# Kernel optimization log

Hardware: AMD Instinct MI355X
Metric: run time of the kernel (lower is better)

The kernel has to match this reference:

```python
import jax, jax.numpy as jnp
import numpy as np

N_NODES = 100000
D_FEAT = 128
N_EDGES = 1500000
H1 = 2 * D_FEAT  # 256, input to first linear (concat of src/dst feats)
H2 = 128


def setup_inputs() -> dict:
    key = jax.random.key(0)
    k_x, k_e, k_w1, k_w2 = jax.random.split(key, 4)
    x = jax.random.normal(k_x, (N_NODES, D_FEAT), dtype=jnp.float32)
    edge_label_index = jax.random.randint(k_e, (2, N_EDGES), 0, N_NODES, dtype=jnp.int64)
    # Kaiming-ish small init for stability
    W1 = jax.random.normal(k_w1, (H1, H2), dtype=jnp.float32) * (1.0 / np.sqrt(H1))
    b1 = jnp.zeros((H2,), dtype=jnp.float32)
    W2 = jax.random.normal(k_w2, (H2, 1), dtype=jnp.float32) * (1.0 / np.sqrt(H2))
    b2 = jnp.zeros((1,), dtype=jnp.float32)
    return {"x": x, "edge_label_index": edge_label_index,
            "W1": W1, "b1": b1, "W2": W2, "b2": b2}


def reference(x, edge_label_index, W1, b1, W2, b2):
    row, col = edge_label_index[0], edge_label_index[1]
    # gather node pair features and concat: [E, 2*D]
    h = jnp.concatenate([x[row], x[col]], axis=-1)
    h = jax.nn.relu(h @ W1 + b1)  # [E, H2]
    out = h @ W2 + b2             # [E, 1]
    return out.reshape(-1)        # [E]
```

## Files before the change

### kernel.cpp

```cpp
#include <hip/hip_runtime.h>
#include <hip/hip_bf16.h>
#include <stdint.h>

typedef __attribute__((ext_vector_type(8))) short s16x8;
typedef __attribute__((ext_vector_type(8))) unsigned short u16x8;
typedef __attribute__((ext_vector_type(4))) float f32x4;

#define D_FEAT 128
#define H2 128
#define BLOCK_THREADS 512
#define WAVES 8
#define MW 32
#define EDGES_PER_BLOCK (WAVES * MW)

__device__ __forceinline__ unsigned short f2bf(float f) {
  uint32_t u = __float_as_uint(f);
  return (unsigned short)((u + 0x7fffu + ((u >> 16) & 1u)) >> 16);
}

__global__ void k_cvt_x(const float* __restrict__ x, unsigned short* __restrict__ xb, int n8) {
  int i = blockIdx.x * blockDim.x + threadIdx.x;
  if (i >= n8) return;
  const f32x4* p = (const f32x4*)x + (size_t)i * 2;
  f32x4 a = p[0], b = p[1];
  u16x8 o;
  o[0] = f2bf(a[0]); o[1] = f2bf(a[1]); o[2] = f2bf(a[2]); o[3] = f2bf(a[3]);
  o[4] = f2bf(b[0]); o[5] = f2bf(b[1]); o[6] = f2bf(b[2]); o[7] = f2bf(b[3]);
  ((u16x8*)xb)[i] = o;
}

__global__ void k_cvt_w1(const float* __restrict__ W1, unsigned short* __restrict__ w1t) {
  int tid = blockIdx.x * blockDim.x + threadIdx.x;
  int chunk = tid >> 7;
  int n = tid & 127;
  u16x8 o;
#pragma unroll
  for (int j = 0; j < 8; ++j)
    o[j] = f2bf(W1[(chunk * 8 + j) * H2 + n]);
  *(u16x8*)(w1t + (n << 8) + ((chunk ^ (n & 7)) << 3)) = o;
}

template <bool XBF>
__global__ __launch_bounds__(BLOCK_THREADS, 4)
void k_edge_mlp(const float* __restrict__ xf,
                const unsigned short* __restrict__ xb,
                const int* __restrict__ eli,
                const float* __restrict__ W1,
                const unsigned short* __restrict__ w1ws,
                const float* __restrict__ b1,
                const float* __restrict__ W2,
                const float* __restrict__ b2,
                float* __restrict__ out, int E, int nNodes)
{
  __shared__ unsigned short w1t[H2 * 256];
  const int t    = threadIdx.x;
  const int lane = t & 63;
  const int wid  = t >> 6;
  const int c    = lane & 15;
  const int g    = lane >> 4;

  if (XBF) {
#pragma unroll
    for (int i = 0; i < 8; ++i) {
      int idx = i * BLOCK_THREADS + t;
      ((u16x8*)w1t)[idx] = ((const u16x8*)w1ws)[idx];
    }
  } else {
    int cg = t >> 7;
    int n  = t & 127;
#pragma unroll
    for (int i = 0; i < 8; ++i) {
      int ch = cg + 4 * i;
      u16x8 o;
#pragma unroll
      for (int j = 0; j < 8; ++j)
        o[j] = f2bf(W1[(ch * 8 + j) * H2 + n]);
      *(u16x8*)(w1t + (n << 8) + ((ch ^ (n & 7)) << 3)) = o;
    }
  }

  const int wbase = blockIdx.x * EDGES_PER_BLOCK + wid * MW;
  const unsigned short* pr[2];
  const unsigned short* pc[2];
  const float* prf[2];
  const float* pcf[2];
#pragma unroll
  for (int m = 0; m < 2; ++m) {
    int e = wbase + m * 16 + c;
    e = e < E ? e : E - 1;
    int nr = eli[e];
    int nc = eli[E + e];
    nr = nr < 0 ? 0 : (nr >= nNodes ? nNodes - 1 : nr);
    nc = nc < 0 ? 0 : (nc >= nNodes ? nNodes - 1 : nc);
    if (XBF) {
      pr[m] = xb + (unsigned)nr * D_FEAT + g * 8;
      pc[m] = xb + (unsigned)nc * D_FEAT + g * 8;
    } else {
      prf[m] = xf + (unsigned)nr * D_FEAT + g * 8;
      pcf[m] = xf + (unsigned)nc * D_FEAT + g * 8;
    }
  }

  __syncthreads();

  auto loadA = [&](int kk, s16x8* dst) {
#pragma unroll
    for (int m = 0; m < 2; ++m) {
      if (XBF) {
        const unsigned short* p = (kk < 4 ? pr[m] : pc[m]);
        dst[m] = *(const s16x8*)(p + (kk & 3) * 32);
      } else {
        const float* p = (kk < 4 ? prf[m] : pcf[m]) + (kk & 3) * 32;
        const f32x4* q = (const f32x4*)p;
        f32x4 a = q[0], b = q[1];
        s16x8 v;
        v[0] = (short)f2bf(a[0]); v[1] = (short)f2bf(a[1]);
        v[2] = (short)f2bf(a[2]); v[3] = (short)f2bf(a[3]);
        v[4] = (short)f2bf(b[0]); v[5] = (short)f2bf(b[1]);
        v[6] = (short)f2bf(b[2]); v[7] = (short)f2bf(b[3]);
        dst[m] = v;
      }
    }
  };

  f32x4 acc[2][8];
#pragma unroll
  for (int m = 0; m < 2; ++m)
#pragma unroll
    for (int f = 0; f < 8; ++f) {
      f32x4 z = {0.f, 0.f, 0.f, 0.f};
      acc[m][f] = z;
    }

  s16x8 abuf[2][2];
  loadA(0, abuf[0]);
  loadA(1, abuf[1]);

#pragma unroll
  for (int kk = 0; kk < 8; ++kk) {
    __builtin_amdgcn_s_setprio(1);
#pragma unroll
    for (int f = 0; f < 8; ++f) {
      int n = f * 16 + c;
      s16x8 bfrag = *(const s16x8*)(w1t + (n << 8) + (((kk * 4 + g) ^ (n & 7)) << 3));
#pragma unroll
      for (int m = 0; m < 2; ++m)
        acc[m][f] = __builtin_amdgcn_mfma_f32_16x16x32_bf16(abuf[kk & 1][m], bfrag, acc[m][f], 0, 0, 0);
    }
    __builtin_amdgcn_s_setprio(0);
    if (kk < 6) loadA(kk + 2, abuf[kk & 1]);
  }

  float b1v[8], w2v[8];
#pragma unroll
  for (int f = 0; f < 8; ++f) {
    b1v[f] = b1[f * 16 + c];
    w2v[f] = W2[f * 16 + c];
  }
  const float b2s = b2[0];

#pragma unroll
  for (int m = 0; m < 2; ++m) {
    float sr[4];
#pragma unroll
    for (int r = 0; r < 4; ++r) {
      float s = 0.f;
#pragma unroll
      for (int f = 0; f < 8; ++f) {
        float h = acc[m][f][r] + b1v[f];
        h = h > 0.f ? h : 0.f;
        s += h * w2v[f];
      }
#pragma unroll
      for (int msk = 1; msk < 16; msk <<= 1)
        s += __shfl_xor(s, msk, 64);
      sr[r] = s;
    }
    int ebase = wbase + m * 16 + g * 4;
    if (c == 0 && ebase < E) {
      f32x4 o = {sr[0] + b2s, sr[1] + b2s, sr[2] + b2s, sr[3] + b2s};
      *(f32x4*)(out + ebase) = o;
    }
  }
}

extern "C" void kernel_launch(void* const* d_in, const int* in_sizes, int n_in,
                              void* d_out, int out_size, void* d_ws, size_t ws_size,
                              hipStream_t stream) {
  const float* x   = (const float*)d_in[0];
  const int*   eli = (const int*)d_in[1];
  const float* W1  = (const float*)d_in[2];
  const float* b1  = (const float*)d_in[3];
  const float* W2  = (const float*)d_in[4];
  const float* b2  = (const float*)d_in[5];
  float* out = (float*)d_out;

  const int E      = in_sizes[1] / 2;
  const int nNodes = in_sizes[0] / D_FEAT;

  const size_t xbytes = (size_t)nNodes * D_FEAT * 2;
  const size_t need   = xbytes + 65536;
  const bool bfpath   = (ws_size >= need);

  const int grid = (E + EDGES_PER_BLOCK - 1) / EDGES_PER_BLOCK;

  if (bfpath) {
    unsigned short* xbw  = (unsigned short*)d_ws;
    unsigned short* w1tw = (unsigned short*)((char*)d_ws + xbytes);
    int n8 = nNodes * D_FEAT / 8;
    k_cvt_x<<<(n8 + 255) / 256, 256, 0, stream>>>(x, xbw, n8);
    k_cvt_w1<<<16, 256, 0, stream>>>(W1, w1tw);
    k_edge_mlp<true><<<grid, BLOCK_THREADS, 0, stream>>>(
        x, xbw, eli, W1, w1tw, b1, W2, b2, out, E, nNodes);
  } else {
    k_edge_mlp<false><<<grid, BLOCK_THREADS, 0, stream>>>(
        x, nullptr, eli, W1, nullptr, b1, W2, b2, out, E, nNodes);
  }
}
```

Before: 140.7 us.

## Make edge MLP kernel persistent with cross-tile prefetch of gathered features

Launches a fixed grid of 512 blocks that loop over edge tiles in grid-stride order. W1 is staged into LDS once per block instead of once per tile. The next tile's indices and first feature fragments are prefetched while the current tile's epilogue runs. The B-fragment LDS offsets are precomputed into registers. This raises register pressure and may lower occupancy, and the fixed grid can leave CUs unevenly loaded.

```diff
diff --git a/kernel.cpp b/kernel.cpp
--- a/kernel.cpp
+++ b/kernel.cpp
@@ -11,7 +11,8 @@
 #define BLOCK_THREADS 512
 #define WAVES 8
 #define MW 32
-#define EDGES_PER_BLOCK (WAVES * MW)
+#define EPB (WAVES * MW)
+#define PERSIST_BLOCKS 512
 
 __device__ __forceinline__ unsigned short f2bf(float f) {
   uint32_t u = __float_as_uint(f);
@@ -53,21 +54,22 @@
                 float* __restrict__ out, int E, int nNodes)
 {
   __shared__ unsigned short w1t[H2 * 256];
-  const int t    = threadIdx.x;
-  const int lane = t & 63;
-  const int wid  = t >> 6;
+  const int t0   = threadIdx.x;
+  const int lane = t0 & 63;
+  const int wid  = t0 >> 6;
   const int c    = lane & 15;
   const int g    = lane >> 4;
+  const int ch7  = c & 7;
 
   if (XBF) {
 #pragma unroll
     for (int i = 0; i < 8; ++i) {
-      int idx = i * BLOCK_THREADS + t;
+      int idx = i * BLOCK_THREADS + t0;
       ((u16x8*)w1t)[idx] = ((const u16x8*)w1ws)[idx];
     }
   } else {
-    int cg = t >> 7;
-    int n  = t & 127;
+    int cg = t0 >> 7;
+    int n  = t0 & 127;
 #pragma unroll
     for (int i = 0; i < 8; ++i) {
       int ch = cg + 4 * i;
@@ -79,39 +81,40 @@
     }
   }
 
-  const int wbase = blockIdx.x * EDGES_PER_BLOCK + wid * MW;
-  const unsigned short* pr[2];
-  const unsigned short* pc[2];
-  const float* prf[2];
-  const float* pcf[2];
-#pragma unroll
-  for (int m = 0; m < 2; ++m) {
-    int e = wbase + m * 16 + c;
-    e = e < E ? e : E - 1;
-    int nr = eli[e];
-    int nc = eli[E + e];
-    nr = nr < 0 ? 0 : (nr >= nNodes ? nNodes - 1 : nr);
-    nc = nc < 0 ? 0 : (nc >= nNodes ? nNodes - 1 : nc);
-    if (XBF) {
-      pr[m] = xb + (unsigned)nr * D_FEAT + g * 8;
-      pc[m] = xb + (unsigned)nc * D_FEAT + g * 8;
-    } else {
-      prf[m] = xf + (unsigned)nr * D_FEAT + g * 8;
-      pcf[m] = xf + (unsigned)nc * D_FEAT + g * 8;
-    }
-  }
+  unsigned boff[8];
+#pragma unroll
+  for (int kk = 0; kk < 8; ++kk)
+    boff[kk] = (unsigned)(c * 256 + (((kk * 4 + g) ^ ch7) << 3));
 
   __syncthreads();
 
-  auto loadA = [&](int kk, s16x8* dst) {
+  const int nt = (E + EPB - 1) / EPB;
+  int t = blockIdx.x;
+  if (t >= nt) return;
+  const int stride = gridDim.x;
+
+  auto mkoff = [&](int tt, unsigned* ro, unsigned* co) {
 #pragma unroll
     for (int m = 0; m < 2; ++m) {
+      int e = tt * EPB + wid * MW + m * 16 + c;
+      e = e < E ? e : E - 1;
+      int nr = eli[e];
+      int nc = eli[E + e];
+      nr = nr < 0 ? 0 : (nr >= nNodes ? nNodes - 1 : nr);
+      nc = nc < 0 ? 0 : (nc >= nNodes ? nNodes - 1 : nc);
+      ro[m] = (unsigned)nr * D_FEAT + g * 8;
+      co[m] = (unsigned)nc * D_FEAT + g * 8;
+    }
+  };
+
+  auto loadA = [&](const unsigned* ro, const unsigned* co, int kk, s16x8* dst) {
+#pragma unroll
+    for (int m = 0; m < 2; ++m) {
+      unsigned off = (kk < 4 ? ro[m] : co[m]) + (unsigned)((kk & 3) * 32);
       if (XBF) {
-        const unsigned short* p = (kk < 4 ? pr[m] : pc[m]);
-        dst[m] = *(const s16x8*)(p + (kk & 3) * 32);
+        dst[m] = *(const s16x8*)(xb + off);
       } else {
-        const float* p = (kk < 4 ? prf[m] : pcf[m]) + (kk & 3) * 32;
-        const f32x4* q = (const f32x4*)p;
+        const f32x4* q = (const f32x4*)(xf + off);
         f32x4 a = q[0], b = q[1];
         s16x8 v;
         v[0] = (short)f2bf(a[0]); v[1] = (short)f2bf(a[1]);
@@ -123,64 +126,82 @@
     }
   };
 
-  f32x4 acc[2][8];
-#pragma unroll
-  for (int m = 0; m < 2; ++m)
+  unsigned ro[2], co[2], ron[2], con[2];
+  mkoff(t, ro, co);
+  s16x8 abuf[2][2];
+  loadA(ro, co, 0, abuf[0]);
+  loadA(ro, co, 1, abuf[1]);
+
+  while (true) {
+    const int tn = t + stride;
+    const bool more = (tn < nt);
+    if (more) mkoff(tn, ron, con);
+
+    f32x4 acc[2][8];
+#pragma unroll
+    for (int m = 0; m < 2; ++m)
+#pragma unroll
+      for (int f = 0; f < 8; ++f) {
+        f32x4 z = {0.f, 0.f, 0.f, 0.f};
+        acc[m][f] = z;
+      }
+
+#pragma unroll
+    for (int kk = 0; kk < 8; ++kk) {
+      __builtin_amdgcn_s_setprio(1);
+#pragma unroll
+      for (int f = 0; f < 8; ++f) {
+        s16x8 bfrag = *(const s16x8*)(w1t + boff[kk] + f * 4096);
+#pragma unroll
+        for (int m = 0; m < 2; ++m)
+          acc[m][f] = __builtin_amdgcn_mfma_f32_16x16x32_bf16(abuf[kk & 1][m], bfrag, acc[m][f], 0, 0, 0);
+      }
+      __builtin_amdgcn_s_setprio(0);
+      if (kk < 6) loadA(ro, co, kk + 2, abuf[kk & 1]);
+    }
+
+    if (more) {
+      loadA(ron, con, 0, abuf[0]);
+      loadA(ron, con, 1, abuf[1]);
+    }
+
+    float b1v[8], w2v[8];
 #pragma unroll
     for (int f = 0; f < 8; ++f) {
-      f32x4 z = {0.f, 0.f, 0.f, 0.f};
-      acc[m][f] = z;
-    }
-
-  s16x8 abuf[2][2];
-  loadA(0, abuf[0]);
-  loadA(1, abuf[1]);
-
-#pragma unroll
-  for (int kk = 0; kk < 8; ++kk) {
-    __builtin_amdgcn_s_setprio(1);
-#pragma unroll
-    for (int f = 0; f < 8; ++f) {
-      int n = f * 16 + c;
-      s16x8 bfrag = *(const s16x8*)(w1t + (n << 8) + (((kk * 4 + g) ^ (n & 7)) << 3));
-#pragma unroll
-      for (int m = 0; m < 2; ++m)
-        acc[m][f] = __builtin_amdgcn_mfma_f32_16x16x32_bf16(abuf[kk & 1][m], bfrag, acc[m][f], 0, 0, 0);
-    }
-    __builtin_amdgcn_s_setprio(0);
-    if (kk < 6) loadA(kk + 2, abuf[kk & 1]);
-  }
-
-  float b1v[8], w2v[8];
-#pragma unroll
-  for (int f = 0; f < 8; ++f) {
-    b1v[f] = b1[f * 16 + c];
-    w2v[f] = W2[f * 16 + c];
-  }
-  const float b2s = b2[0];
-
-#pragma unroll
-  for (int m = 0; m < 2; ++m) {
-    float sr[4];
-#pragma unroll
-    for (int r = 0; r < 4; ++r) {
-      float s = 0.f;
-#pragma unroll
-      for (int f = 0; f < 8; ++f) {
-        float h = acc[m][f][r] + b1v[f];
-        h = h > 0.f ? h : 0.f;
-        s += h * w2v[f];
-      }
-#pragma unroll
-      for (int msk = 1; msk < 16; msk <<= 1)
-        s += __shfl_xor(s, msk, 64);
-      sr[r] = s;
-    }
-    int ebase = wbase + m * 16 + g * 4;
-    if (c == 0 && ebase < E) {
-      f32x4 o = {sr[0] + b2s, sr[1] + b2s, sr[2] + b2s, sr[3] + b2s};
-      *(f32x4*)(out + ebase) = o;
-    }
+      b1v[f] = b1[f * 16 + c];
+      w2v[f] = W2[f * 16 + c];
+    }
+    const float b2s = b2[0];
+
+    const int tbase = t * EPB + wid * MW;
+#pragma unroll
+    for (int m = 0; m < 2; ++m) {
+      float sr[4];
+#pragma unroll
+      for (int r = 0; r < 4; ++r) {
+        float s = 0.f;
+#pragma unroll
+        for (int f = 0; f < 8; ++f) {
+          float h = acc[m][f][r] + b1v[f];
+          h = h > 0.f ? h : 0.f;
+          s += h * w2v[f];
+        }
+#pragma unroll
+        for (int msk = 1; msk < 16; msk <<= 1)
+          s += __shfl_xor(s, msk, 64);
+        sr[r] = s;
+      }
+      int ebase = tbase + m * 16 + g * 4;
+      if (c == 0 && ebase < E) {
+        f32x4 o = {sr[0] + b2s, sr[1] + b2s, sr[2] + b2s, sr[3] + b2s};
+        *(f32x4*)(out + ebase) = o;
+      }
+    }
+
+    if (!more) break;
+    t = tn;
+#pragma unroll
+    for (int m = 0; m < 2; ++m) { ro[m] = ron[m]; co[m] = con[m]; }
   }
 }
 
@@ -202,7 +223,8 @@
   const size_t need   = xbytes + 65536;
   const bool bfpath   = (ws_size >= need);
 
-  const int grid = (E + EDGES_PER_BLOCK - 1) / EDGES_PER_BLOCK;
+  const int nt   = (E + EPB - 1) / EPB;
+  const int grid = nt < PERSIST_BLOCKS ? nt : PERSIST_BLOCKS;
 
   if (bfpath) {
     unsigned short* xbw  = (unsigned short*)d_ws;
```

Result: slower. 177.3 us (+26.1%).
